# Kernel tuning notes

Measured on AMD Instinct MI355X. Metric: run time of the kernel, lower is better.

## Reference

```python
import jax, jax.numpy as jnp
import numpy as np

N, D = 8192, 256
NEG_BIG = -9e15


def setup_inputs() -> dict:
    key = jax.random.key(0)
    k1, k2, k3 = jax.random.split(key, 3)
    h = jax.random.normal(k1, (N, D), dtype=jnp.float32)
    adj = jax.random.randint(k2, (N, N), 0, 2, dtype=jnp.int32)
    # xavier_uniform for a of shape (2D, 1): bound = sqrt(6/(2D+1))
    bound = np.sqrt(6.0 / (2 * D + 1)).astype(np.float32)
    a = jax.random.uniform(k3, (2 * D, 1), dtype=jnp.float32, minval=-bound, maxval=bound)
    return {"h": h, "adj": adj, "a": a}


def reference(h, adj, a):
    d = h.shape[1]
    h1 = h @ a[:d]            # [N, 1]
    h2 = h @ a[d:]            # [N, 1]
    e = jax.nn.leaky_relu(h1 + h2.T, negative_slope=0.01)  # [N, N]
    attention = jnp.where(adj > 0, e, NEG_BIG)
    attention = jax.nn.softmax(attention, axis=1)
    # dropout skipped: eval mode (training=False)
    return attention @ h      # [N, D]
```

## Files before the change

kernel.cpp:

```cpp
#include <hip/hip_runtime.h>
#include <hip/hip_bf16.h>

#define NTOT 8192
#define DDIM 256
#define ROWS 32
#define JCHUNK (NTOT / 8)
#define NITER (JCHUNK / 32)
#define NWORDS (NTOT / 32)

typedef __attribute__((ext_vector_type(8))) short short8;
typedef __attribute__((ext_vector_type(4))) float floatx4;

__global__ __launch_bounds__(256) void gat_scores(const float* __restrict__ h,
                                                  const float* __restrict__ a,
                                                  float* __restrict__ s1,
                                                  float* __restrict__ s2) {
  int row  = blockIdx.x * 4 + (threadIdx.x >> 6);
  int lane = threadIdx.x & 63;
  const float* hr = h + (size_t)row * DDIM;
  float p1 = 0.f, p2 = 0.f;
#pragma unroll
  for (int k = 0; k < DDIM / 64; ++k) {
    int idx  = lane + 64 * k;
    float hv = hr[idx];
    p1 += hv * a[idx];
    p2 += hv * a[DDIM + idx];
  }
#pragma unroll
  for (int off = 32; off > 0; off >>= 1) {
    p1 += __shfl_down(p1, off, 64);
    p2 += __shfl_down(p2, off, 64);
  }
  if (lane == 0) { s1[row] = p1; s2[row] = p2; }
}

__global__ __launch_bounds__(256) void gat_pack(const int* __restrict__ adj,
                                                unsigned* __restrict__ bitsT) {
  __shared__ unsigned words[64][65];
  const int t    = threadIdx.x;
  const int lane = t & 63;
  const int w    = t >> 6;
  const int r0   = blockIdx.x * 64;
  const int jb   = blockIdx.y * 2048;

#pragma unroll 2
  for (int rr = 0; rr < 16; ++rr) {
    const int rl = w * 16 + rr;
    const int* ap = adj + (size_t)(r0 + rl) * NTOT + jb + lane * 4;
#pragma unroll
    for (int R = 0; R < 8; ++R) {
      int4 v = *(const int4*)(ap + R * 256);
      unsigned nib = (v.x > 0 ? 1u : 0u) | (v.y > 0 ? 2u : 0u) |
                     (v.z > 0 ? 4u : 0u) | (v.w > 0 ? 8u : 0u);
      unsigned b8  = nib | (__shfl_xor((int)nib, 1, 64) << 4);
      unsigned b16 = b8  | (__shfl_xor((int)b8,  2, 64) << 8);
      unsigned b32 = b16 | (__shfl_xor((int)b16, 4, 64) << 16);
      if ((lane & 7) == 0) words[rl][R * 8 + (lane >> 3)] = b32;
    }
  }
  __syncthreads();

#pragma unroll 4
  for (int kk = 0; kk < 16; ++kk) {
    const int jwl = w * 16 + kk;
    bitsT[(size_t)(jb / 32 + jwl) * NTOT + r0 + lane] = words[lane][jwl];
  }
}

__global__ __launch_bounds__(256) void gat_hpack(const float* __restrict__ h,
                                                 ushort* __restrict__ hTf) {
  __shared__ float tile[64][257];
  const int t    = threadIdx.x;
  const int lane = t & 63;
  const int w    = t >> 6;
  const int quad = lane >> 4;
  const int c    = lane & 15;
  const int i0   = blockIdx.x * 64;

#pragma unroll
  for (int it = 0; it < 16; ++it) {
    int r = it * 4 + w;
    float4 v = *(const float4*)(h + (size_t)(i0 + r) * DDIM + lane * 4);
    tile[r][lane * 4 + 0] = v.x; tile[r][lane * 4 + 1] = v.y;
    tile[r][lane * 4 + 2] = v.z; tile[r][lane * 4 + 3] = v.w;
  }
  __syncthreads();

#pragma unroll
  for (int k = 0; k < 4; ++k) {
    const int n = 4 * k + w;
#pragma unroll
    for (int jbl = 0; jbl < 2; ++jbl) {
      short8 vv;
#pragma unroll
      for (int i = 0; i < 8; ++i) {
        float f = tile[jbl * 32 + quad * 8 + i][n * 16 + c];
        __hip_bfloat16 b = __float2bfloat16(f);
        vv[i] = *(short*)&b;
      }
      *(short8*)(hTf + ((size_t)(n * 256 + i0 / 32 + jbl) * 64 + lane) * 8) = vv;
    }
  }
}

__global__ __launch_bounds__(512, 2) void gat_attn(const ushort* __restrict__ hTf,
                                                   const unsigned* __restrict__ bitsT,
                                                   const float* __restrict__ s1g,
                                                   const float* __restrict__ s2g,
                                                   float* __restrict__ out) {
  __shared__ union {
    float lred[8][32];
    float slab[4][ROWS * 128];
  } sh;

  const int t    = threadIdx.x;
  const int lane = t & 63;
  const int w    = t >> 6;
  const int quad = lane >> 4;
  const int c    = lane & 15;
  const int r0   = blockIdx.x * ROWS;

  const float s10 = s1g[r0 + c];
  const float s11 = s1g[r0 + 16 + c];

  const unsigned* btp = bitsT + (size_t)(w * 32) * NTOT;
  const float*    s2p = s2g + w * JCHUNK + 8 * quad;
  const ushort*   hfp = hTf + (size_t)(w * 32) * 512 + lane * 8;

  floatx4 acc[2][16];
#pragma unroll
  for (int rt = 0; rt < 2; ++rt)
#pragma unroll
    for (int nt = 0; nt < 16; ++nt) acc[rt][nt] = (floatx4){0.f, 0.f, 0.f, 0.f};

  float lp0 = 0.f, lp1 = 0.f;

  unsigned W0 = btp[r0 + c];
  unsigned W1 = btp[r0 + 16 + c];
  float4 sa = ((const float4*)s2p)[0];
  float4 sb = ((const float4*)s2p)[1];

  for (int jt = 0; jt < NITER; ++jt) {
    short8 bfr[16];
    const ushort* hp = hfp + (size_t)jt * 512;
#pragma unroll
    for (int nt = 0; nt < 16; ++nt)
      bfr[nt] = *(const short8*)(hp + (size_t)nt * 131072);

    const unsigned bm0 = (W0 >> (quad * 8)) & 0xff;
    const unsigned bm1 = (W1 >> (quad * 8)) & 0xff;
    float sv[8] = {sa.x, sa.y, sa.z, sa.w, sb.x, sb.y, sb.z, sb.w};
    short8 pa0, pa1;
#pragma unroll
    for (int i = 0; i < 8; ++i) {
      float e0 = s10 + sv[i];
      e0 = fmaxf(e0, 0.01f * e0);
      float p0 = ((bm0 >> i) & 1) ? __expf(e0) : 0.f;
      lp0 += p0;
      __hip_bfloat16 b0 = __float2bfloat16(p0);
      pa0[i] = *(short*)&b0;
      float e1 = s11 + sv[i];
      e1 = fmaxf(e1, 0.01f * e1);
      float p1 = ((bm1 >> i) & 1) ? __expf(e1) : 0.f;
      lp1 += p1;
      __hip_bfloat16 b1 = __float2bfloat16(p1);
      pa1[i] = *(short*)&b1;
    }

    if (jt + 1 < NITER) {
      W0 = btp[(size_t)(jt + 1) * NTOT + r0 + c];
      W1 = btp[(size_t)(jt + 1) * NTOT + r0 + 16 + c];
      sa = ((const float4*)(s2p + (jt + 1) * 32))[0];
      sb = ((const float4*)(s2p + (jt + 1) * 32))[1];
    }

#pragma unroll
    for (int nt = 0; nt < 16; ++nt) {
      acc[0][nt] = __builtin_amdgcn_mfma_f32_16x16x32_bf16(pa0, bfr[nt], acc[0][nt], 0, 0, 0);
      acc[1][nt] = __builtin_amdgcn_mfma_f32_16x16x32_bf16(pa1, bfr[nt], acc[1][nt], 0, 0, 0);
    }
  }

  lp0 += __shfl_xor(lp0, 16, 64); lp0 += __shfl_xor(lp0, 32, 64);
  lp1 += __shfl_xor(lp1, 16, 64); lp1 += __shfl_xor(lp1, 32, 64);
  if (quad == 0) { sh.lred[w][c] = lp0; sh.lred[w][16 + c] = lp1; }
  __syncthreads();

  float linv[2][4];
  if (w == 0) {
#pragma unroll
    for (int rt = 0; rt < 2; ++rt)
#pragma unroll
      for (int reg = 0; reg < 4; ++reg) {
        int lrow = rt * 16 + quad * 4 + reg;
        float s = 0.f;
#pragma unroll
        for (int wi = 0; wi < 8; ++wi) s += sh.lred[wi][lrow];
        linv[rt][reg] = 1.f / s;
      }
  }
  __syncthreads();

#pragma unroll
  for (int hd = 0; hd < 2; ++hd) {
    if (w >= 4) {
#pragma unroll
      for (int rt = 0; rt < 2; ++rt)
#pragma unroll
        for (int i = 0; i < 8; ++i)
#pragma unroll
          for (int reg = 0; reg < 4; ++reg)
            sh.slab[w - 4][(rt * 16 + quad * 4 + reg) * 128 + i * 16 + c] =
                acc[rt][i + 8 * hd][reg];
    }
    __syncthreads();
    if (w < 4) {
#pragma unroll
      for (int rt = 0; rt < 2; ++rt)
#pragma unroll
        for (int i = 0; i < 8; ++i)
#pragma unroll
          for (int reg = 0; reg < 4; ++reg)
            acc[rt][i + 8 * hd][reg] +=
                sh.slab[w][(rt * 16 + quad * 4 + reg) * 128 + i * 16 + c];
    }
    __syncthreads();
    if (w == 2 || w == 3) {
#pragma unroll
      for (int rt = 0; rt < 2; ++rt)
#pragma unroll
        for (int i = 0; i < 8; ++i)
#pragma unroll
          for (int reg = 0; reg < 4; ++reg)
            sh.slab[w - 2][(rt * 16 + quad * 4 + reg) * 128 + i * 16 + c] =
                acc[rt][i + 8 * hd][reg];
    }
    __syncthreads();
    if (w < 2) {
#pragma unroll
      for (int rt = 0; rt < 2; ++rt)
#pragma unroll
        for (int i = 0; i < 8; ++i)
#pragma unroll
          for (int reg = 0; reg < 4; ++reg)
            acc[rt][i + 8 * hd][reg] +=
                sh.slab[w][(rt * 16 + quad * 4 + reg) * 128 + i * 16 + c];
    }
    __syncthreads();
    if (w == 1) {
#pragma unroll
      for (int rt = 0; rt < 2; ++rt)
#pragma unroll
        for (int i = 0; i < 8; ++i)
#pragma unroll
          for (int reg = 0; reg < 4; ++reg)
            sh.slab[0][(rt * 16 + quad * 4 + reg) * 128 + i * 16 + c] =
                acc[rt][i + 8 * hd][reg];
    }
    __syncthreads();
    if (w == 0) {
#pragma unroll
      for (int rt = 0; rt < 2; ++rt)
#pragma unroll
        for (int i = 0; i < 8; ++i)
#pragma unroll
          for (int reg = 0; reg < 4; ++reg) {
            float v = acc[rt][i + 8 * hd][reg] +
                      sh.slab[0][(rt * 16 + quad * 4 + reg) * 128 + i * 16 + c];
            out[(size_t)(r0 + rt * 16 + quad * 4 + reg) * DDIM +
                hd * 128 + i * 16 + c] = v * linv[rt][reg];
          }
    }
    __syncthreads();
  }
}

extern "C" void kernel_launch(void* const* d_in, const int* in_sizes, int n_in,
                              void* d_out, int out_size, void* d_ws, size_t ws_size,
                              hipStream_t stream) {
  const float* h   = (const float*)d_in[0];
  const int*   adj = (const int*)d_in[1];
  const float* a   = (const float*)d_in[2];
  float* out = (float*)d_out;

  float*    s1    = (float*)d_ws;
  float*    s2    = s1 + NTOT;
  unsigned* bitsT = (unsigned*)(s2 + NTOT);
  ushort*   hTf   = (ushort*)(bitsT + (size_t)NWORDS * NTOT);

  gat_scores<<<NTOT / 4, 256, 0, stream>>>(h, a, s1, s2);
  gat_pack<<<dim3(NTOT / 64, 4), 256, 0, stream>>>(adj, bitsT);
  gat_hpack<<<NTOT / 64, 256, 0, stream>>>(h, hTf);
  gat_attn<<<NTOT / ROWS, 512, 0, stream>>>(hTf, bitsT, s1, s2, out);
}
```

Measured before the change: 454.2 us.

## Factor exp of leaky-relu scores into per-row/col tables and double-buffer B loads

Replaces the per-element exp of leaky_relu(s1+s2) with products of precomputed exponentials: exp(s1)*exp(s2) when s1+s2>0, otherwise exp(0.01 s1)*exp(0.01 s2), chosen by comparing exp(s2) against exp(-s1). This removes the transcendental from the inner attention loop. It also splits the h fragment loads into two halves so the next tile's first half loads while the second half's MFMAs run, and pads the per-column stride of the packed h layout, presumably to spread memory channel or bank conflicts. The factored exponentials can overflow or underflow differently from the direct form for large scores, and the extra buffers add register pressure.

```diff
diff --git a/kernel.cpp b/kernel.cpp
--- a/kernel.cpp
+++ b/kernel.cpp
@@ -7,6 +7,7 @@
 #define JCHUNK (NTOT / 8)
 #define NITER (JCHUNK / 32)
 #define NWORDS (NTOT / 32)
+#define NTSTR 131584
 
 typedef __attribute__((ext_vector_type(8))) short short8;
 typedef __attribute__((ext_vector_type(4))) float floatx4;
@@ -14,7 +15,9 @@
 __global__ __launch_bounds__(256) void gat_scores(const float* __restrict__ h,
                                                   const float* __restrict__ a,
                                                   float* __restrict__ s1,
-                                                  float* __restrict__ s2) {
+                                                  float* __restrict__ s2,
+                                                  float4* __restrict__ rc,
+                                                  float2* __restrict__ etab) {
   int row  = blockIdx.x * 4 + (threadIdx.x >> 6);
   int lane = threadIdx.x & 63;
   const float* hr = h + (size_t)row * DDIM;
@@ -31,7 +34,11 @@
     p1 += __shfl_down(p1, off, 64);
     p2 += __shfl_down(p2, off, 64);
   }
-  if (lane == 0) { s1[row] = p1; s2[row] = p2; }
+  if (lane == 0) {
+    s1[row] = p1; s2[row] = p2;
+    rc[row]   = make_float4(__expf(p1), __expf(0.01f * p1), __expf(-p1), 0.f);
+    etab[row] = make_float2(__expf(p2), __expf(0.01f * p2));
+  }
 }
 
 __global__ __launch_bounds__(256) void gat_pack(const int* __restrict__ adj,
@@ -98,15 +105,15 @@
         __hip_bfloat16 b = __float2bfloat16(f);
         vv[i] = *(short*)&b;
       }
-      *(short8*)(hTf + ((size_t)(n * 256 + i0 / 32 + jbl) * 64 + lane) * 8) = vv;
+      *(short8*)(hTf + ((size_t)(n * 257 + i0 / 32 + jbl) * 64 + lane) * 8) = vv;
     }
   }
 }
 
 __global__ __launch_bounds__(512, 2) void gat_attn(const ushort* __restrict__ hTf,
                                                    const unsigned* __restrict__ bitsT,
-                                                   const float* __restrict__ s1g,
-                                                   const float* __restrict__ s2g,
+                                                   const float4* __restrict__ rc,
+                                                   const float2* __restrict__ etab,
                                                    float* __restrict__ out) {
   __shared__ union {
     float lred[8][32];
@@ -120,12 +127,14 @@
   const int c    = lane & 15;
   const int r0   = blockIdx.x * ROWS;
 
-  const float s10 = s1g[r0 + c];
-  const float s11 = s1g[r0 + 16 + c];
+  const float4 rc0 = rc[r0 + c];
+  const float4 rc1 = rc[r0 + 16 + c];
+  const float E10 = rc0.x, E20 = rc0.y, T0 = rc0.z;
+  const float E11 = rc1.x, E21 = rc1.y, T1 = rc1.z;
 
   const unsigned* btp = bitsT + (size_t)(w * 32) * NTOT;
-  const float*    s2p = s2g + w * JCHUNK + 8 * quad;
-  const ushort*   hfp = hTf + (size_t)(w * 32) * 512 + lane * 8;
+  const float*    etb = (const float*)(etab + (size_t)w * JCHUNK + quad * 8);
+  const ushort*   hfp = hTf + ((size_t)(w * 32) * 64 + lane) * 8;
 
   floatx4 acc[2][16];
 #pragma unroll
@@ -134,52 +143,68 @@
     for (int nt = 0; nt < 16; ++nt) acc[rt][nt] = (floatx4){0.f, 0.f, 0.f, 0.f};
 
   float lp0 = 0.f, lp1 = 0.f;
-
+  short8 bA[8], bB[8];
+
+  #define LDH(dst, jt, half)                                                   \
+    _Pragma("unroll")                                                          \
+    for (int q = 0; q < 8; ++q)                                                \
+      dst[q] = *(const short8*)(hfp + (size_t)(jt) * 512 +                     \
+                                (size_t)((half) * 8 + q) * NTSTR);
+
+  LDH(bA, 0, 0)
   unsigned W0 = btp[r0 + c];
   unsigned W1 = btp[r0 + 16 + c];
-  float4 sa = ((const float4*)s2p)[0];
-  float4 sb = ((const float4*)s2p)[1];
+  float4 ea = ((const float4*)etb)[0];
+  float4 eb = ((const float4*)etb)[1];
+  float4 ec = ((const float4*)etb)[2];
+  float4 ed = ((const float4*)etb)[3];
 
   for (int jt = 0; jt < NITER; ++jt) {
-    short8 bfr[16];
-    const ushort* hp = hfp + (size_t)jt * 512;
-#pragma unroll
-    for (int nt = 0; nt < 16; ++nt)
-      bfr[nt] = *(const short8*)(hp + (size_t)nt * 131072);
+    LDH(bB, jt, 1)
 
     const unsigned bm0 = (W0 >> (quad * 8)) & 0xff;
     const unsigned bm1 = (W1 >> (quad * 8)) & 0xff;
-    float sv[8] = {sa.x, sa.y, sa.z, sa.w, sb.x, sb.y, sb.z, sb.w};
+    float tp[16] = {ea.x, ea.y, ea.z, ea.w, eb.x, eb.y, eb.z, eb.w,
+                    ec.x, ec.y, ec.z, ec.w, ed.x, ed.y, ed.z, ed.w};
     short8 pa0, pa1;
 #pragma unroll
     for (int i = 0; i < 8; ++i) {
-      float e0 = s10 + sv[i];
-      e0 = fmaxf(e0, 0.01f * e0);
-      float p0 = ((bm0 >> i) & 1) ? __expf(e0) : 0.f;
-      lp0 += p0;
+      const float t1 = tp[2 * i], t2 = tp[2 * i + 1];
+      const float m0 = (float)((bm0 >> i) & 1u);
+      const float m1 = (float)((bm1 >> i) & 1u);
+      float p0 = ((t1 > T0) ? E10 * t1 : E20 * t2) * m0;
+      float p1 = ((t1 > T1) ? E11 * t1 : E21 * t2) * m1;
+      lp0 += p0; lp1 += p1;
       __hip_bfloat16 b0 = __float2bfloat16(p0);
+      __hip_bfloat16 b1 = __float2bfloat16(p1);
       pa0[i] = *(short*)&b0;
-      float e1 = s11 + sv[i];
-      e1 = fmaxf(e1, 0.01f * e1);
-      float p1 = ((bm1 >> i) & 1) ? __expf(e1) : 0.f;
-      lp1 += p1;
-      __hip_bfloat16 b1 = __float2bfloat16(p1);
       pa1[i] = *(short*)&b1;
     }
 
     if (jt + 1 < NITER) {
       W0 = btp[(size_t)(jt + 1) * NTOT + r0 + c];
       W1 = btp[(size_t)(jt + 1) * NTOT + r0 + 16 + c];
-      sa = ((const float4*)(s2p + (jt + 1) * 32))[0];
-      sb = ((const float4*)(s2p + (jt + 1) * 32))[1];
-    }
-
-#pragma unroll
-    for (int nt = 0; nt < 16; ++nt) {
-      acc[0][nt] = __builtin_amdgcn_mfma_f32_16x16x32_bf16(pa0, bfr[nt], acc[0][nt], 0, 0, 0);
-      acc[1][nt] = __builtin_amdgcn_mfma_f32_16x16x32_bf16(pa1, bfr[nt], acc[1][nt], 0, 0, 0);
-    }
-  }
+      const float* en = etb + (jt + 1) * 64;
+      ea = ((const float4*)en)[0];
+      eb = ((const float4*)en)[1];
+      ec = ((const float4*)en)[2];
+      ed = ((const float4*)en)[3];
+    }
+
+#pragma unroll
+    for (int q = 0; q < 8; ++q) {
+      acc[0][q] = __builtin_amdgcn_mfma_f32_16x16x32_bf16(pa0, bA[q], acc[0][q], 0, 0, 0);
+      acc[1][q] = __builtin_amdgcn_mfma_f32_16x16x32_bf16(pa1, bA[q], acc[1][q], 0, 0, 0);
+    }
+    if (jt + 1 < NITER) { LDH(bA, jt + 1, 0) }
+
+#pragma unroll
+    for (int q = 0; q < 8; ++q) {
+      acc[0][8 + q] = __builtin_amdgcn_mfma_f32_16x16x32_bf16(pa0, bB[q], acc[0][8 + q], 0, 0, 0);
+      acc[1][8 + q] = __builtin_amdgcn_mfma_f32_16x16x32_bf16(pa1, bB[q], acc[1][8 + q], 0, 0, 0);
+    }
+  }
+  #undef LDH
 
   lp0 += __shfl_xor(lp0, 16, 64); lp0 += __shfl_xor(lp0, 32, 64);
   lp1 += __shfl_xor(lp1, 16, 64); lp1 += __shfl_xor(lp1, 32, 64);
@@ -285,11 +310,13 @@
 
   float*    s1    = (float*)d_ws;
   float*    s2    = s1 + NTOT;
-  unsigned* bitsT = (unsigned*)(s2 + NTOT);
+  float4*   rc    = (float4*)(s2 + NTOT);
+  float2*   etab  = (float2*)(rc + NTOT);
+  unsigned* bitsT = (unsigned*)(etab + NTOT);
   ushort*   hTf   = (ushort*)(bitsT + (size_t)NWORDS * NTOT);
 
-  gat_scores<<<NTOT / 4, 256, 0, stream>>>(h, a, s1, s2);
+  gat_scores<<<NTOT / 4, 256, 0, stream>>>(h, a, s1, s2, rc, etab);
   gat_pack<<<dim3(NTOT / 64, 4), 256, 0, stream>>>(adj, bitsT);
   gat_hpack<<<NTOT / 64, 256, 0, stream>>>(h, hTf);
-  gat_attn<<<NTOT / ROWS, 512, 0, stream>>>(hTf, bitsT, s1, s2, out);
-}
+  gat_attn<<<NTOT / ROWS, 512, 0, stream>>>(hTf, bitsT, rc, etab, out);
+}
```

Result: no change. 454.0 us (-0.1%).

## Share LDS-staged h tiles across waves, split j across blocks, precompute exp factors

Applied to the files above, without the earlier changes.

The attention kernel is reorganised so each block covers 256 rows with 8 waves. Each wave owns 32 rows, and all waves share one double-buffered LDS copy of the bf16 h tile, filled by async global_load_lds. Previously each wave loaded its own B fragments from global memory and the block ran an in-block cross-wave reduction. The j dimension is now split across blockIdx.y, with partial sums and denominators written to a workspace and combined by a new reduce kernel. The exponentials are factored into per-row and per-column precomputed exp tables, which removes per-element __expf; for leaky_relu it uses a threshold compare with exp(-s1). This trades a large partial-sum write and read (about 64MB) for reduced global B traffic and cheaper softmax arithmetic. There is some overflow risk from exp of unshifted scores.

```diff
diff --git a/kernel.cpp b/kernel.cpp
--- a/kernel.cpp
+++ b/kernel.cpp
@@ -3,9 +3,11 @@
 
 #define NTOT 8192
 #define DDIM 256
-#define ROWS 32
-#define JCHUNK (NTOT / 8)
-#define NITER (JCHUNK / 32)
+#define NRB 256
+#define JB 32
+#define JSPLIT 8
+#define JCHUNK (NTOT / JSPLIT)
+#define NITER (JCHUNK / JB)
 #define NWORDS (NTOT / 32)
 
 typedef __attribute__((ext_vector_type(8))) short short8;
@@ -13,8 +15,8 @@
 
 __global__ __launch_bounds__(256) void gat_scores(const float* __restrict__ h,
                                                   const float* __restrict__ a,
-                                                  float* __restrict__ s1,
-                                                  float* __restrict__ s2) {
+                                                  float4* __restrict__ rc,
+                                                  float2* __restrict__ etab) {
   int row  = blockIdx.x * 4 + (threadIdx.x >> 6);
   int lane = threadIdx.x & 63;
   const float* hr = h + (size_t)row * DDIM;
@@ -31,7 +33,10 @@
     p1 += __shfl_down(p1, off, 64);
     p2 += __shfl_down(p2, off, 64);
   }
-  if (lane == 0) { s1[row] = p1; s2[row] = p2; }
+  if (lane == 0) {
+    rc[row]   = make_float4(__expf(p1), __expf(0.01f * p1), __expf(-p1), 0.f);
+    etab[row] = make_float2(__expf(p2), __expf(0.01f * p2));
+  }
 }
 
 __global__ __launch_bounds__(256) void gat_pack(const int* __restrict__ adj,
@@ -98,181 +103,144 @@
         __hip_bfloat16 b = __float2bfloat16(f);
         vv[i] = *(short*)&b;
       }
-      *(short8*)(hTf + ((size_t)(n * 256 + i0 / 32 + jbl) * 64 + lane) * 8) = vv;
+      *(short8*)(hTf + ((size_t)(n * 257 + i0 / 32 + jbl) * 64 + lane) * 8) = vv;
     }
   }
 }
 
 __global__ __launch_bounds__(512, 2) void gat_attn(const ushort* __restrict__ hTf,
                                                    const unsigned* __restrict__ bitsT,
-                                                   const float* __restrict__ s1g,
-                                                   const float* __restrict__ s2g,
-                                                   float* __restrict__ out) {
-  __shared__ union {
-    float lred[8][32];
-    float slab[4][ROWS * 128];
-  } sh;
+                                                   const float4* __restrict__ rc,
+                                                   const float2* __restrict__ etab,
+                                                   float* __restrict__ part,
+                                                   float* __restrict__ lpart) {
+  __shared__ ushort Bt[2][16][512];
 
   const int t    = threadIdx.x;
   const int lane = t & 63;
   const int w    = t >> 6;
   const int quad = lane >> 4;
   const int c    = lane & 15;
-  const int r0   = blockIdx.x * ROWS;
-
-  const float s10 = s1g[r0 + c];
-  const float s11 = s1g[r0 + 16 + c];
-
-  const unsigned* btp = bitsT + (size_t)(w * 32) * NTOT;
-  const float*    s2p = s2g + w * JCHUNK + 8 * quad;
-  const ushort*   hfp = hTf + (size_t)(w * 32) * 512 + lane * 8;
+  const int bx   = blockIdx.x;
+  const int by   = blockIdx.y;
+  const int rbase = bx * NRB + w * 32;
+  const int jbase = by * JCHUNK;
+  const int jb32  = jbase / 32;
+
+  const float4 rc0 = rc[rbase + c];
+  const float4 rc1 = rc[rbase + 16 + c];
+  const float E10 = rc0.x, E20 = rc0.y, T0 = rc0.z;
+  const float E11 = rc1.x, E21 = rc1.y, T1 = rc1.z;
 
   floatx4 acc[2][16];
 #pragma unroll
   for (int rt = 0; rt < 2; ++rt)
 #pragma unroll
     for (int nt = 0; nt < 16; ++nt) acc[rt][nt] = (floatx4){0.f, 0.f, 0.f, 0.f};
-
   float lp0 = 0.f, lp1 = 0.f;
 
-  unsigned W0 = btp[r0 + c];
-  unsigned W1 = btp[r0 + 16 + c];
-  float4 sa = ((const float4*)s2p)[0];
-  float4 sb = ((const float4*)s2p)[1];
+#pragma unroll
+  for (int q = 0; q < 2; ++q) {
+    const int nt = 2 * w + q;
+    const ushort* gsrc = hTf + (size_t)(nt * 257 + jb32) * 512 + lane * 8;
+    __builtin_amdgcn_global_load_lds(
+        (const __attribute__((address_space(1))) void*)gsrc,
+        (__attribute__((address_space(3))) void*)&Bt[0][nt][0], 16, 0, 0);
+  }
+  unsigned W0 = bitsT[(size_t)jb32 * NTOT + rbase + c];
+  unsigned W1 = bitsT[(size_t)jb32 * NTOT + rbase + 16 + c];
+  const float* etp = (const float*)etab + ((size_t)jbase + quad * 8) * 2;
+  float4 f0 = ((const float4*)etp)[0];
+  float4 f1 = ((const float4*)etp)[1];
+  float4 f2 = ((const float4*)etp)[2];
+  float4 f3 = ((const float4*)etp)[3];
 
   for (int jt = 0; jt < NITER; ++jt) {
-    short8 bfr[16];
-    const ushort* hp = hfp + (size_t)jt * 512;
-#pragma unroll
-    for (int nt = 0; nt < 16; ++nt)
-      bfr[nt] = *(const short8*)(hp + (size_t)nt * 131072);
-
-    const unsigned bm0 = (W0 >> (quad * 8)) & 0xff;
-    const unsigned bm1 = (W1 >> (quad * 8)) & 0xff;
-    float sv[8] = {sa.x, sa.y, sa.z, sa.w, sb.x, sb.y, sb.z, sb.w};
+    const int p = jt & 1;
+    __syncthreads();
+
+    if (jt + 1 < NITER) {
+#pragma unroll
+      for (int q = 0; q < 2; ++q) {
+        const int nt = 2 * w + q;
+        const ushort* gsrc =
+            hTf + (size_t)(nt * 257 + jb32 + jt + 1) * 512 + lane * 8;
+        __builtin_amdgcn_global_load_lds(
+            (const __attribute__((address_space(1))) void*)gsrc,
+            (__attribute__((address_space(3))) void*)&Bt[p ^ 1][nt][0], 16, 0, 0);
+      }
+    }
+
+    const unsigned bm0 = (W0 >> (quad * 8)) & 0xffu;
+    const unsigned bm1 = (W1 >> (quad * 8)) & 0xffu;
     short8 pa0, pa1;
-#pragma unroll
-    for (int i = 0; i < 8; ++i) {
-      float e0 = s10 + sv[i];
-      e0 = fmaxf(e0, 0.01f * e0);
-      float p0 = ((bm0 >> i) & 1) ? __expf(e0) : 0.f;
-      lp0 += p0;
-      __hip_bfloat16 b0 = __float2bfloat16(p0);
-      pa0[i] = *(short*)&b0;
-      float e1 = s11 + sv[i];
-      e1 = fmaxf(e1, 0.01f * e1);
-      float p1 = ((bm1 >> i) & 1) ? __expf(e1) : 0.f;
-      lp1 += p1;
-      __hip_bfloat16 b1 = __float2bfloat16(p1);
-      pa1[i] = *(short*)&b1;
-    }
+#define PB(i, ex, ey)                                                   \
+    {                                                                   \
+      const float mm0 = (float)((bm0 >> (i)) & 1u);                     \
+      const float mm1 = (float)((bm1 >> (i)) & 1u);                     \
+      float p0v = (((ex) > T0) ? E10 * (ex) : E20 * (ey)) * mm0;        \
+      float p1v = (((ex) > T1) ? E11 * (ex) : E21 * (ey)) * mm1;        \
+      lp0 += p0v; lp1 += p1v;                                           \
+      __hip_bfloat16 q0 = __float2bfloat16(p0v);                        \
+      __hip_bfloat16 q1 = __float2bfloat16(p1v);                        \
+      pa0[i] = *(short*)&q0; pa1[i] = *(short*)&q1;                     \
+    }
+    PB(0, f0.x, f0.y) PB(1, f0.z, f0.w)
+    PB(2, f1.x, f1.y) PB(3, f1.z, f1.w)
+    PB(4, f2.x, f2.y) PB(5, f2.z, f2.w)
+    PB(6, f3.x, f3.y) PB(7, f3.z, f3.w)
+#undef PB
 
     if (jt + 1 < NITER) {
-      W0 = btp[(size_t)(jt + 1) * NTOT + r0 + c];
-      W1 = btp[(size_t)(jt + 1) * NTOT + r0 + 16 + c];
-      sa = ((const float4*)(s2p + (jt + 1) * 32))[0];
-      sb = ((const float4*)(s2p + (jt + 1) * 32))[1];
-    }
-
+      const size_t jw = (size_t)(jb32 + jt + 1);
+      W0 = bitsT[jw * NTOT + rbase + c];
+      W1 = bitsT[jw * NTOT + rbase + 16 + c];
+      const float* en = etp + (size_t)(jt + 1) * 64;
+      f0 = ((const float4*)en)[0];
+      f1 = ((const float4*)en)[1];
+      f2 = ((const float4*)en)[2];
+      f3 = ((const float4*)en)[3];
+    }
+
+    const ushort* bb = &Bt[p][0][lane * 8];
 #pragma unroll
     for (int nt = 0; nt < 16; ++nt) {
-      acc[0][nt] = __builtin_amdgcn_mfma_f32_16x16x32_bf16(pa0, bfr[nt], acc[0][nt], 0, 0, 0);
-      acc[1][nt] = __builtin_amdgcn_mfma_f32_16x16x32_bf16(pa1, bfr[nt], acc[1][nt], 0, 0, 0);
+      short8 bfr = *(const short8*)(bb + nt * 512);
+      acc[0][nt] = __builtin_amdgcn_mfma_f32_16x16x32_bf16(pa0, bfr, acc[0][nt], 0, 0, 0);
+      acc[1][nt] = __builtin_amdgcn_mfma_f32_16x16x32_bf16(pa1, bfr, acc[1][nt], 0, 0, 0);
     }
   }
 
   lp0 += __shfl_xor(lp0, 16, 64); lp0 += __shfl_xor(lp0, 32, 64);
   lp1 += __shfl_xor(lp1, 16, 64); lp1 += __shfl_xor(lp1, 32, 64);
-  if (quad == 0) { sh.lred[w][c] = lp0; sh.lred[w][16 + c] = lp1; }
-  __syncthreads();
-
-  float linv[2][4];
-  if (w == 0) {
-#pragma unroll
-    for (int rt = 0; rt < 2; ++rt)
-#pragma unroll
-      for (int reg = 0; reg < 4; ++reg) {
-        int lrow = rt * 16 + quad * 4 + reg;
-        float s = 0.f;
-#pragma unroll
-        for (int wi = 0; wi < 8; ++wi) s += sh.lred[wi][lrow];
-        linv[rt][reg] = 1.f / s;
-      }
-  }
-  __syncthreads();
-
-#pragma unroll
-  for (int hd = 0; hd < 2; ++hd) {
-    if (w >= 4) {
-#pragma unroll
-      for (int rt = 0; rt < 2; ++rt)
-#pragma unroll
-        for (int i = 0; i < 8; ++i)
-#pragma unroll
-          for (int reg = 0; reg < 4; ++reg)
-            sh.slab[w - 4][(rt * 16 + quad * 4 + reg) * 128 + i * 16 + c] =
-                acc[rt][i + 8 * hd][reg];
-    }
-    __syncthreads();
-    if (w < 4) {
-#pragma unroll
-      for (int rt = 0; rt < 2; ++rt)
-#pragma unroll
-        for (int i = 0; i < 8; ++i)
-#pragma unroll
-          for (int reg = 0; reg < 4; ++reg)
-            acc[rt][i + 8 * hd][reg] +=
-                sh.slab[w][(rt * 16 + quad * 4 + reg) * 128 + i * 16 + c];
-    }
-    __syncthreads();
-    if (w == 2 || w == 3) {
-#pragma unroll
-      for (int rt = 0; rt < 2; ++rt)
-#pragma unroll
-        for (int i = 0; i < 8; ++i)
-#pragma unroll
-          for (int reg = 0; reg < 4; ++reg)
-            sh.slab[w - 2][(rt * 16 + quad * 4 + reg) * 128 + i * 16 + c] =
-                acc[rt][i + 8 * hd][reg];
-    }
-    __syncthreads();
-    if (w < 2) {
-#pragma unroll
-      for (int rt = 0; rt < 2; ++rt)
-#pragma unroll
-        for (int i = 0; i < 8; ++i)
-#pragma unroll
-          for (int reg = 0; reg < 4; ++reg)
-            acc[rt][i + 8 * hd][reg] +=
-                sh.slab[w][(rt * 16 + quad * 4 + reg) * 128 + i * 16 + c];
-    }
-    __syncthreads();
-    if (w == 1) {
-#pragma unroll
-      for (int rt = 0; rt < 2; ++rt)
-#pragma unroll
-        for (int i = 0; i < 8; ++i)
-#pragma unroll
-          for (int reg = 0; reg < 4; ++reg)
-            sh.slab[0][(rt * 16 + quad * 4 + reg) * 128 + i * 16 + c] =
-                acc[rt][i + 8 * hd][reg];
-    }
-    __syncthreads();
-    if (w == 0) {
-#pragma unroll
-      for (int rt = 0; rt < 2; ++rt)
-#pragma unroll
-        for (int i = 0; i < 8; ++i)
-#pragma unroll
-          for (int reg = 0; reg < 4; ++reg) {
-            float v = acc[rt][i + 8 * hd][reg] +
-                      sh.slab[0][(rt * 16 + quad * 4 + reg) * 128 + i * 16 + c];
-            out[(size_t)(r0 + rt * 16 + quad * 4 + reg) * DDIM +
-                hd * 128 + i * 16 + c] = v * linv[rt][reg];
-          }
-    }
-    __syncthreads();
-  }
+  if (quad == 0) {
+    lpart[(size_t)by * NTOT + rbase + c]      = lp0;
+    lpart[(size_t)by * NTOT + rbase + 16 + c] = lp1;
+  }
+  float* pp = part + ((size_t)by * NTOT + rbase) * DDIM;
+#pragma unroll
+  for (int rt = 0; rt < 2; ++rt)
+#pragma unroll
+    for (int nt = 0; nt < 16; ++nt)
+#pragma unroll
+      for (int reg = 0; reg < 4; ++reg)
+        pp[(size_t)(rt * 16 + quad * 4 + reg) * DDIM + nt * 16 + c] =
+            acc[rt][nt][reg];
+}
+
+__global__ __launch_bounds__(256) void gat_reduce(const float* __restrict__ part,
+                                                  const float* __restrict__ lpart,
+                                                  float* __restrict__ out) {
+  const int row = blockIdx.x;
+  const int t   = threadIdx.x;
+  float l = 0.f;
+#pragma unroll
+  for (int js = 0; js < JSPLIT; ++js) l += lpart[(size_t)js * NTOT + row];
+  float s = 0.f;
+#pragma unroll
+  for (int js = 0; js < JSPLIT; ++js)
+    s += part[((size_t)js * NTOT + row) * DDIM + t];
+  out[(size_t)row * DDIM + t] = s / l;
 }
 
 extern "C" void kernel_launch(void* const* d_in, const int* in_sizes, int n_in,
@@ -282,14 +250,18 @@
   const int*   adj = (const int*)d_in[1];
   const float* a   = (const float*)d_in[2];
   float* out = (float*)d_out;
-
-  float*    s1    = (float*)d_ws;
-  float*    s2    = s1 + NTOT;
-  unsigned* bitsT = (unsigned*)(s2 + NTOT);
-  ushort*   hTf   = (ushort*)(bitsT + (size_t)NWORDS * NTOT);
-
-  gat_scores<<<NTOT / 4, 256, 0, stream>>>(h, a, s1, s2);
+  char* ws = (char*)d_ws;
+
+  float4*   rc    = (float4*)(ws);
+  float2*   etab  = (float2*)(ws + (128 << 10));
+  unsigned* bitsT = (unsigned*)(ws + (1 << 20));
+  ushort*   hTf   = (ushort*)(ws + (10 << 20));
+  float*    part  = (float*)(ws + (16 << 20));
+  float*    lpart = (float*)(ws + (82 << 20));
+
+  gat_scores<<<NTOT / 4, 256, 0, stream>>>(h, a, rc, etab);
   gat_pack<<<dim3(NTOT / 64, 4), 256, 0, stream>>>(adj, bitsT);
   gat_hpack<<<NTOT / 64, 256, 0, stream>>>(h, hTf);
-  gat_attn<<<NTOT / ROWS, 512, 0, stream>>>(hTf, bitsT, s1, s2, out);
-}
+  gat_attn<<<dim3(NTOT / NRB, JSPLIT), 512, 0, stream>>>(hTf, bitsT, rc, etab, part, lpart);
+  gat_reduce<<<NTOT, 256, 0, stream>>>(part, lpart, out);
+}
```

Measured after the change: 472.7 us. 4.1% more time.
